# Optimization experiments

Measured on AMD Instinct MI355X. Metric: run time of the kernel, lower is better.

## Reference

```python
import jax, jax.numpy as jnp
import numpy as np

B, V, T, F, H = 32, 16, 64, 64, 512
NBINS = 36  # 360 / delta (delta_cog = delta_rb = 10)
OUT = 4     # output_size


def setup_inputs() -> dict:
    key = jax.random.key(0)
    ks = jax.random.split(key, 12)
    s = 1.0 / np.sqrt(H)
    return {
        'sequence': jax.random.normal(ks[0], (B, V, T, F), jnp.float32),
        'dist_matrix': jax.random.uniform(ks[1], (B, V, T, V), jnp.float32),
        'rb_matrix': jax.random.randint(ks[2], (B, V, T, V), 0, NBINS).astype(jnp.int32),
        'cog_matrix': jax.random.randint(ks[3], (B, V, T, V), 0, NBINS).astype(jnp.int32),
        'seq_mask': jnp.ones((B, V, T), jnp.float32),
        'maxval': jax.random.uniform(ks[4], (B, F), jnp.float32) + 1.0,
        'minval': jax.random.uniform(ks[5], (B, F), jnp.float32),
        # per-vessel LSTMCell params (PyTorch gate order i,f,g,o stacked along 4H)
        'W_ih': jax.random.normal(ks[6], (V, 4 * H, F), jnp.float32) * s,
        'W_hh': jax.random.normal(ks[7], (V, 4 * H, H), jnp.float32) * s,
        'b_ih': jnp.zeros((V, 4 * H), jnp.float32),
        'b_hh': jnp.zeros((V, 4 * H), jnp.float32),
        # hardwired attention domain table [360/delta_cog, 360/delta_rb]
        'domain': jax.random.normal(ks[8], (NBINS, NBINS), jnp.float32),
        # per-vessel softAttention linear (2H -> H)
        'soft_W': jax.random.normal(ks[9], (V, H, 2 * H), jnp.float32) * s,
        'soft_b': jnp.zeros((V, H), jnp.float32),
        # shared output linear (H -> F)
        'out_W': jax.random.normal(ks[10], (F, H), jnp.float32) * s,
        'out_b': jnp.zeros((F,), jnp.float32),
    }


def _forward(sequence, dist_matrix, rb_matrix, cog_matrix, seq_mask, maxval, minval,
             W_ih, W_hh, b_ih, b_hh, domain, soft_W, soft_b, out_W, out_b):
    B_, V_, T_, F_ = sequence.shape
    H_ = W_hh.shape[-1]

    def hardwired(h, r, d, m, cg):
        # h: [B,V,H]; r,d,cg: [B,V,V]; m: [B,V]
        mul1 = m[:, :, None] * m[:, None, :]
        mul2 = domain[cg, r]
        w = jax.nn.relu(mul2 - d) * mul1
        w = w / jax.lax.stop_gradient(jnp.max(w))  # torch: weights /= weights.data.max()
        return jnp.einsum('bvw,bwh->bvh', w, h)

    def lstm_step(x, h, c):
        # vectorized over V independent LSTMCells
        g = (jnp.einsum('bvf,vgf->bvg', x, W_ih)
             + jnp.einsum('bvh,vgh->bvg', h, W_hh) + b_ih + b_hh)
        i, f, gg, o = jnp.split(g, 4, axis=-1)
        c_new = jax.nn.sigmoid(f) * c + jax.nn.sigmoid(i) * jnp.tanh(gg)
        h_new = jax.nn.sigmoid(o) * jnp.tanh(c_new)
        return h_new, c_new

    h0 = jnp.zeros((B_, V_, H_), sequence.dtype)
    c0 = jnp.zeros((B_, V_, H_), sequence.dtype)
    xs = (jnp.moveaxis(sequence, 2, 0), jnp.moveaxis(rb_matrix, 2, 0),
          jnp.moveaxis(dist_matrix, 2, 0), jnp.moveaxis(seq_mask, 2, 0),
          jnp.moveaxis(cog_matrix, 2, 0))

    def enc_step(carry, xt):
        h, c = carry
        x, r, d, m, cg = xt
        wh = hardwired(h, r, d, m, cg)
        h, c = lstm_step(x, wh, c)
        return (h, c), h

    (h, c), enc = jax.lax.scan(enc_step, (h0, c0), xs)
    enc = jnp.moveaxis(enc, 0, 2)  # encodedInput [B,V,T,H]

    # decoder, prediction step i=0 (prediction_length=1)
    wh = hardwired(h, rb_matrix[:, :, -1], dist_matrix[:, :, -1],
                   seq_mask[:, :, -1], cog_matrix[:, :, -1])
    # get_previous_sequence: denormalize under no_grad
    prev = jax.lax.stop_gradient(
        sequence[:, :, -1] * (maxval - minval)[:, None, :] + minval[:, None, :])
    h, c = lstm_step(prev, wh, c)

    # per-vessel softAttention
    score = jnp.einsum('bvth,bvh->bvt', enc, h)
    alpha = jax.nn.softmax(score * seq_mask, axis=-1)
    ctx = jnp.einsum('bvt,bvth->bvh', alpha, enc)
    # faithful to torch.stack((ctx, h)).view(B, 2H) memory-reinterpret per vessel
    z = jnp.moveaxis(jnp.stack([ctx, h], axis=0), 2, 0).reshape(V_, B_, 2 * H_)
    h = jnp.moveaxis(
        jnp.tanh(jnp.einsum('vbk,vhk->vbh', z, soft_W) + soft_b[:, None, :]), 0, 1)

    out = jax.nn.relu(jnp.einsum('bvh,fh->bvf', h, out_W) + out_b)
    return out[:, :, None, :OUT]  # [B, V, prediction_length=1, output_size]


def reference(sequence, dist_matrix, rb_matrix, cog_matrix, seq_mask, maxval, minval,
              W_ih, W_hh, b_ih, b_hh, domain, soft_W, soft_b, out_W, out_b,
              maxVessels=V):
    return _forward(sequence, dist_matrix, rb_matrix, cog_matrix, seq_mask,
                    maxval, minval, W_ih, W_hh, b_ih, b_hh, domain,
                    soft_W, soft_b, out_W, out_b)
```

## Files before the change

kernel.cpp:

```cpp
#include <hip/hip_runtime.h>
#include <math.h>

#define B 32
#define V 16
#define T 64
#define F 64
#define H 512
#define NB 36
#define G4H 2048

typedef unsigned short u16;
typedef unsigned long long ull;
typedef __attribute__((ext_vector_type(8))) short bf16x8;
typedef __attribute__((ext_vector_type(4))) float f32x4;

#define OFF_H0     0
#define OFF_H1     262144
#define OFF_C      524288
#define OFF_CNT    786432
#define OFF_WALL   794624
#define OFF_CTX    794624
#define OFF_HSOFT  1056768
#define OFF_WMAX   1318912
#define OFF_WHSTG  1318976
#define OFF_SEQSTG 1581120
#define OFF_WSTG   2646080
#define OFF_ENC    12083264

#define WHP 262144
#define WLDS_BYTES 147456

__device__ __forceinline__ float sigmoidf_(float x) { return 1.0f / (1.0f + __expf(-x)); }

__device__ __forceinline__ u16 f2bf(float f) {
    union { float f; unsigned u; } x; x.f = f;
    unsigned r = x.u + 0x7FFF + ((x.u >> 16) & 1);
    return (u16)(r >> 16);
}
__device__ __forceinline__ float bf2f(u16 u) {
    union { unsigned i; float f; } x; x.i = ((unsigned)u) << 16;
    return x.f;
}
__device__ __forceinline__ f32x4 mfma16(bf16x8 a, bf16x8 b, f32x4 c) {
    return __builtin_amdgcn_mfma_f32_16x16x32_bf16(a, b, c, 0, 0, 0);
}
__device__ __forceinline__ bf16x8 mk_bf16x8(ull lo, ull hi) {
    union { ull u[2]; bf16x8 v; } x; x.u[0] = lo; x.u[1] = hi; return x.v;
}
__device__ __forceinline__ bf16x8 mk_bf16x8q(uint4 q) {
    union { uint4 q; bf16x8 v; } x; x.q = q; return x.v;
}

__device__ __forceinline__ ull ld_agent(const ull* p) {
    return __hip_atomic_load((ull*)p, __ATOMIC_RELAXED, __HIP_MEMORY_SCOPE_AGENT);
}
__device__ __forceinline__ void st_agent(ull* p, ull x) {
    __hip_atomic_store(p, x, __ATOMIC_RELAXED, __HIP_MEMORY_SCOPE_AGENT);
}
__device__ __forceinline__ void st_agent_f(float* p, float x) {
    __hip_atomic_store(p, x, __ATOMIC_RELAXED, __HIP_MEMORY_SCOPE_AGENT);
}
__device__ __forceinline__ void st_agent_u32(unsigned* p, unsigned x) {
    __hip_atomic_store(p, x, __ATOMIC_RELAXED, __HIP_MEMORY_SCOPE_AGENT);
}
__device__ __forceinline__ unsigned ld_agent_u32(const unsigned* p) {
    return __hip_atomic_load((unsigned*)p, __ATOMIC_RELAXED, __HIP_MEMORY_SCOPE_AGENT);
}

__global__ void k_zero(float* __restrict__ p, int n) {
    int i = blockIdx.x * blockDim.x + threadIdx.x;
    if (i < n) p[i] = 0.0f;
}

__global__ __launch_bounds__(256) void k_hw_all(
    const float* __restrict__ dist, const int* __restrict__ rb,
    const int* __restrict__ cog, const float* __restrict__ mask,
    const float* __restrict__ domain, float* __restrict__ w_all,
    float* __restrict__ wmax_all) {
    int t = blockIdx.x;
    __shared__ float red[256];
    int tid = threadIdx.x;
    float lmax = 0.0f;
    for (int idx = tid; idx < B * V * V; idx += 256) {
        int b = idx >> 8;
        int rem = idx & 255;
        int i = rem >> 4, j = rem & 15;
        int base = ((b * V + i) * T + t) * V + j;
        float val = domain[cog[base] * NB + rb[base]] - dist[base];
        val = val > 0.0f ? val : 0.0f;
        val *= mask[(b * V + i) * T + t] * mask[(b * V + j) * T + t];
        w_all[t * (B * V * V) + idx] = val;
        lmax = fmaxf(lmax, val);
    }
    red[tid] = lmax;
    __syncthreads();
    for (int s = 128; s > 0; s >>= 1) {
        if (tid < s) red[tid] = fmaxf(red[tid], red[tid + s]);
        __syncthreads();
    }
    if (tid == 0) wmax_all[t] = red[0];
}

__global__ __launch_bounds__(256) void k_wconv(
    const float* __restrict__ W_ih, const float* __restrict__ W_hh,
    u16* __restrict__ Wstg) {
    int v = blockIdx.x, hk = blockIdx.y, ks = blockIdx.z;
    int tid = threadIdx.x;
#pragma unroll
    for (int s = 0; s < 2; ++s) {
        int slot = tid + s * 256;
        int nt = slot >> 6, lane = slot & 63;
        int g = nt >> 1, hh = nt & 1;
        int col = g * H + hk * 32 + hh * 16 + (lane & 15);
        int k = ks * 32 + ((lane >> 4) << 3);
        const float* src = (k < F) ? &W_ih[(v * G4H + col) * F + k]
                                   : &W_hh[(v * G4H + col) * H + (k - F)];
        float4 x0 = *(const float4*)src;
        float4 x1 = *(const float4*)(src + 4);
        union { u16 u[8]; uint4 q; } pk;
        pk.u[0] = f2bf(x0.x); pk.u[1] = f2bf(x0.y); pk.u[2] = f2bf(x0.z); pk.u[3] = f2bf(x0.w);
        pk.u[4] = f2bf(x1.x); pk.u[5] = f2bf(x1.y); pk.u[6] = f2bf(x1.z); pk.u[7] = f2bf(x1.w);
        *(uint4*)&Wstg[(size_t)((((v * 16 + hk) * 18 + ks) * 8 + nt) * 64 + lane) * 8] = pk.q;
    }
}

__global__ __launch_bounds__(256) void k_seqstg(
    const float* __restrict__ seq, const float* __restrict__ maxval,
    const float* __restrict__ minval, u16* __restrict__ seqstg) {
    int v = blockIdx.x, t = blockIdx.y;
    int tid = threadIdx.x;
    int mt = tid >> 7, ks = (tid >> 6) & 1, lane = tid & 63;
    int b = mt * 16 + (lane & 15);
    int f = ks * 32 + ((lane >> 4) << 3);
    union { u16 u[8]; uint4 q; } pk;
    if (t < T) {
        const float* sp = &seq[((b * V + v) * T + t) * F + f];
        float4 x0 = *(const float4*)sp, x1 = *(const float4*)(sp + 4);
        pk.u[0] = f2bf(x0.x); pk.u[1] = f2bf(x0.y); pk.u[2] = f2bf(x0.z); pk.u[3] = f2bf(x0.w);
        pk.u[4] = f2bf(x1.x); pk.u[5] = f2bf(x1.y); pk.u[6] = f2bf(x1.z); pk.u[7] = f2bf(x1.w);
    } else {
        const float* sp = &seq[((b * V + v) * T + (T - 1)) * F + f];
        float4 x0 = *(const float4*)sp, x1 = *(const float4*)(sp + 4);
        float4 mx0 = *(const float4*)&maxval[b * F + f], mx1 = *(const float4*)&maxval[b * F + f + 4];
        float4 mn0 = *(const float4*)&minval[b * F + f], mn1 = *(const float4*)&minval[b * F + f + 4];
        pk.u[0] = f2bf(x0.x * (mx0.x - mn0.x) + mn0.x);
        pk.u[1] = f2bf(x0.y * (mx0.y - mn0.y) + mn0.y);
        pk.u[2] = f2bf(x0.z * (mx0.z - mn0.z) + mn0.z);
        pk.u[3] = f2bf(x0.w * (mx0.w - mn0.w) + mn0.w);
        pk.u[4] = f2bf(x1.x * (mx1.x - mn1.x) + mn1.x);
        pk.u[5] = f2bf(x1.y * (mx1.y - mn1.y) + mn1.y);
        pk.u[6] = f2bf(x1.z * (mx1.z - mn1.z) + mn1.z);
        pk.u[7] = f2bf(x1.w * (mx1.w - mn1.w) + mn1.w);
    }
    *(uint4*)&seqstg[(((size_t)(t * 16 + v)) * 4 + mt * 2 + ks) * 512 + lane * 8] = pk.q;
}

__global__ __launch_bounds__(256) void k_recur(
    const u16* __restrict__ seqstg, const u16* __restrict__ Wstg,
    const float* __restrict__ w_all, const float* __restrict__ wmax_all,
    const float* __restrict__ b_ih, const float* __restrict__ b_hh,
    float* __restrict__ h0buf, float* __restrict__ h1buf,
    float* __restrict__ c, u16* __restrict__ enc, u16* __restrict__ whstg,
    unsigned* __restrict__ bar) {
    extern __shared__ u16 Wlds[];

    int bid = blockIdx.x;
    int v = bid & 15, hk = bid >> 4;
    int tid = threadIdx.x;

    {
        const uint4* wsrc = (const uint4*)(Wstg + (size_t)((v * 16 + hk) * 18) * 4096);
        uint4* wdst = (uint4*)Wlds;
        for (int i = tid; i < 9216; i += 256) wdst[i] = wsrc[i];
    }

    int lane = tid & 63, wvi = tid >> 6;
    int mtw = wvi & 1, hh = wvi >> 1;
    int col = hk * 32 + hh * 16 + (lane & 15);
    int q4 = (lane >> 4) << 2;
    float bi = b_ih[v * G4H + col] + b_hh[v * G4H + col];
    float bf_ = b_ih[v * G4H + H + col] + b_hh[v * G4H + H + col];
    float bg_ = b_ih[v * G4H + 2 * H + col] + b_hh[v * G4H + 2 * H + col];
    float bo = b_ih[v * G4H + 3 * H + col] + b_hh[v * G4H + 3 * H + col];

    unsigned* aslot = bar + (v * 16 + hk) * 16;
    unsigned* bslot = bar + (256 + hk * 16 + v) * 16;
    unsigned* apoll = bar + (v * 16 + (tid & 15)) * 16;
    unsigned* bpoll = bar + (256 + hk * 16 + (tid & 15)) * 16;

    int a_b = tid >> 3;
    int a_cq = tid & 7;
    const int wh_idx = ((((v * 2 + (a_b >> 4)) * 16 + hk) * 64 +
                         (((a_cq >> 1) << 4) + (a_b & 15))) * 8 + (a_cq & 1) * 4);

    __syncthreads();

    for (int t = 0; t <= T; ++t) {
        int par = t & 1;
        int tm = t < T ? t : (T - 1);
        const float* hin = (t & 1) ? h0buf : h1buf;
        float* hout = (t & 1) ? h1buf : h0buf;

        uint4 s0 = *(const uint4*)&seqstg[(((size_t)(t * 16 + v)) * 4 + mtw * 2 + 0) * 512 + lane * 8];
        uint4 s1 = *(const uint4*)&seqstg[(((size_t)(t * 16 + v)) * 4 + mtw * 2 + 1) * 512 + lane * 8];
        float inv = 1.0f / wmax_all[tm];
        const float* wrow = &w_all[(size_t)tm * (B * V * V) + (a_b * V + v) * V];
        float4 wr0 = *(const float4*)(wrow);
        float4 wr1 = *(const float4*)(wrow + 4);
        float4 wr2 = *(const float4*)(wrow + 8);
        float4 wr3 = *(const float4*)(wrow + 12);
        float cprev[4];
#pragma unroll
        for (int r = 0; r < 4; ++r)
            cprev[r] = c[((mtw * 16 + q4 + r) * V + v) * H + col];

        f32x4 acc[4];
        acc[0][0] = bi;  acc[0][1] = bi;  acc[0][2] = bi;  acc[0][3] = bi;
        acc[1][0] = bf_; acc[1][1] = bf_; acc[1][2] = bf_; acc[1][3] = bf_;
        acc[2][0] = bg_; acc[2][1] = bg_; acc[2][2] = bg_; acc[2][3] = bg_;
        acc[3][0] = bo;  acc[3][1] = bo;  acc[3][2] = bo;  acc[3][3] = bo;
        {
            bf16x8 a0f = mk_bf16x8q(s0);
            bf16x8 a1f = mk_bf16x8q(s1);
#pragma unroll
            for (int g = 0; g < 4; ++g)
                acc[g] = mfma16(a0f, *(const bf16x8*)&Wlds[(0 * 8 + (g * 2 + hh)) * 512 + lane * 8], acc[g]);
#pragma unroll
            for (int g = 0; g < 4; ++g)
                acc[g] = mfma16(a1f, *(const bf16x8*)&Wlds[(1 * 8 + (g * 2 + hh)) * 512 + lane * 8], acc[g]);
        }

        if (t > 0) {
            if (tid < 16) {
                while (ld_agent_u32(bpoll) < (unsigned)t) __builtin_amdgcn_s_sleep(1);
            }
            __syncthreads();
        }

        {
            const ull* hb = (const ull*)&hin[(a_b * V) * H + hk * 32 + a_cq * 4];
            float a0 = 0.f, a1 = 0.f, a2 = 0.f, a3 = 0.f;
            const float wj[16] = {wr0.x, wr0.y, wr0.z, wr0.w, wr1.x, wr1.y, wr1.z, wr1.w,
                                  wr2.x, wr2.y, wr2.z, wr2.w, wr3.x, wr3.y, wr3.z, wr3.w};
#pragma unroll
            for (int j = 0; j < 16; ++j) {
                ull lo = ld_agent(hb + (size_t)j * (H / 2));
                ull hi = ld_agent(hb + (size_t)j * (H / 2) + 1);
                union { ull u; float f[2]; } u0, u1;
                u0.u = lo; u1.u = hi;
                a0 = fmaf(wj[j], u0.f[0], a0);
                a1 = fmaf(wj[j], u0.f[1], a1);
                a2 = fmaf(wj[j], u1.f[0], a2);
                a3 = fmaf(wj[j], u1.f[1], a3);
            }
            union { u16 u[4]; ull q; } pk;
            pk.u[0] = f2bf(a0 * inv); pk.u[1] = f2bf(a1 * inv);
            pk.u[2] = f2bf(a2 * inv); pk.u[3] = f2bf(a3 * inv);
            st_agent((ull*)&whstg[par * WHP + wh_idx], pk.q);
        }
        __syncthreads();
        if (tid == 0) st_agent_u32(aslot, (unsigned)(t + 1));

        if (tid < 16) {
            while (ld_agent_u32(apoll) < (unsigned)(t + 1)) __builtin_amdgcn_s_sleep(1);
        }
        __syncthreads();

        bf16x8 afr[16];
#pragma unroll
        for (int ksw = 0; ksw < 16; ++ksw) {
            const ull* src = (const ull*)&whstg[par * WHP + (((v * 2 + mtw) * 16 + ksw) * 64 + lane) * 8];
            ull lo = ld_agent(src), hi = ld_agent(src + 1);
            afr[ksw] = mk_bf16x8(lo, hi);
        }
#pragma unroll
        for (int ks = 0; ks < 16; ++ks) {
#pragma unroll
            for (int g = 0; g < 4; ++g) {
                bf16x8 wfr = *(const bf16x8*)&Wlds[((ks + 2) * 8 + (g * 2 + hh)) * 512 + lane * 8];
                acc[g] = mfma16(afr[ks], wfr, acc[g]);
            }
        }

        float cnv[4], hnv[4];
#pragma unroll
        for (int r = 0; r < 4; ++r) {
            float gi = acc[0][r];
            float gf = acc[1][r];
            float gg = acc[2][r];
            float go = acc[3][r];
            cnv[r] = sigmoidf_(gf) * cprev[r] + sigmoidf_(gi) * tanhf(gg);
            hnv[r] = sigmoidf_(go) * tanhf(cnv[r]);
            int b = mtw * 16 + q4 + r;
            st_agent_f(&hout[(b * V + v) * H + col], hnv[r]);
        }
        if (t < T) {
            __syncthreads();
            if (tid == 0) st_agent_u32(bslot, (unsigned)(t + 1));
        }

#pragma unroll
        for (int r = 0; r < 4; ++r) {
            int b = mtw * 16 + q4 + r;
            c[((b * V + v)) * H + col + 0 * H * V] = cnv[r];
            if (t < T) enc[((size_t)(b * V + v) * T + t) * H + col] = f2bf(hnv[r]);
        }
    }
}

__global__ __launch_bounds__(256) void k_attn(
    const u16* __restrict__ enc, const float* __restrict__ h,
    const float* __restrict__ mask, float* __restrict__ ctx) {
    int bid = blockIdx.x;
    int b = bid >> 4, v = bid & 15;
    int tid = threadIdx.x;
    int wave = tid >> 6, lane = tid & 63;
    __shared__ float hs[H];
    __shared__ float sc[T];
    __shared__ float al[T];
    const u16* encbase = enc + (size_t)((b * V + v) * T) * H;
    const float* hb = h + (b * V + v) * H;
    for (int i = tid; i < H; i += 256) hs[i] = hb[i];
    __syncthreads();
    for (int tt = wave; tt < T; tt += 4) {
        const u16* e = encbase + tt * H;
        float p = 0.0f;
#pragma unroll
        for (int ii = 0; ii < 8; ++ii) p += bf2f(e[ii * 64 + lane]) * hs[ii * 64 + lane];
        for (int off = 32; off; off >>= 1) p += __shfl_down(p, off, 64);
        if (lane == 0) sc[tt] = p;
    }
    __syncthreads();
    if (tid < 64) {
        float m_t = mask[(b * V + v) * T + tid];
        float s = sc[tid] * m_t;
        float mx = s;
        for (int off = 32; off; off >>= 1) mx = fmaxf(mx, __shfl_xor(mx, off, 64));
        float e = __expf(s - mx);
        float sum = e;
        for (int off = 32; off; off >>= 1) sum += __shfl_xor(sum, off, 64);
        al[tid] = e / sum;
    }
    __syncthreads();
    for (int hh = tid; hh < H; hh += 256) {
        float a = 0.0f;
        for (int tt = 0; tt < T; ++tt) a += al[tt] * bf2f(encbase[tt * H + hh]);
        ctx[(b * V + v) * H + hh] = a;
    }
}

__global__ __launch_bounds__(256) void k_soft(
    const float* __restrict__ ctx, const float* __restrict__ hdec,
    const float* __restrict__ soft_W, const float* __restrict__ soft_b,
    float* __restrict__ hsoft) {
    int v = blockIdx.x;
    int h0 = blockIdx.y * 32;
    int tid = threadIdx.x;
    int cg = tid & 31, rg = tid >> 5;
    __shared__ float sA[32][36];
    __shared__ float sW2[32][36];
    float* sAf = &sA[0][0];
    float* sWf = &sW2[0][0];
    float acc[4] = {0.f, 0.f, 0.f, 0.f};
    int arow = tid >> 3, akq = tid & 7;
    float4 areg, wreg;

    {
        int k = akq * 4;
        const float* src = (arow < 16) ? ctx : hdec;
        int bsrc = 2 * (arow & 15) + (k >= H ? 1 : 0);
        areg = *(const float4*)&src[(bsrc * V + v) * H + (k & (H - 1))];
        wreg = *(const float4*)&soft_W[(v * H + h0 + arow) * (2 * H) + k];
    }
    for (int kc = 0; kc < 2 * H; kc += 32) {
        __syncthreads();
        *(float4*)&sAf[arow * 36 + akq * 4] = areg;
        *(float4*)&sWf[arow * 36 + akq * 4] = wreg;
        __syncthreads();
        if (kc + 32 < 2 * H) {
            int k = kc + 32 + akq * 4;
            const float* src = (arow < 16) ? ctx : hdec;
            int bsrc = 2 * (arow & 15) + (k >= H ? 1 : 0);
            areg = *(const float4*)&src[(bsrc * V + v) * H + (k & (H - 1))];
            wreg = *(const float4*)&soft_W[(v * H + h0 + arow) * (2 * H) + kc + 32 + akq * 4];
        }
#pragma unroll
        for (int k4 = 0; k4 < 8; ++k4) {
            float4 wv = *(const float4*)&sWf[cg * 36 + k4 * 4];
            float4 a0 = *(const float4*)&sAf[(rg * 4 + 0) * 36 + k4 * 4];
            float4 a1 = *(const float4*)&sAf[(rg * 4 + 1) * 36 + k4 * 4];
            float4 a2 = *(const float4*)&sAf[(rg * 4 + 2) * 36 + k4 * 4];
            float4 a3 = *(const float4*)&sAf[(rg * 4 + 3) * 36 + k4 * 4];
            acc[0] += a0.x * wv.x + a0.y * wv.y + a0.z * wv.z + a0.w * wv.w;
            acc[1] += a1.x * wv.x + a1.y * wv.y + a1.z * wv.z + a1.w * wv.w;
            acc[2] += a2.x * wv.x + a2.y * wv.y + a2.z * wv.z + a2.w * wv.w;
            acc[3] += a3.x * wv.x + a3.y * wv.y + a3.z * wv.z + a3.w * wv.w;
        }
    }
    float bb = soft_b[v * H + h0 + cg];
#pragma unroll
    for (int r = 0; r < 4; ++r) {
        int row = rg * 4 + r;
        hsoft[(row * V + v) * H + h0 + cg] = tanhf(acc[r] + bb);
    }
}

__global__ __launch_bounds__(64) void k_out(
    const float* __restrict__ hsoft, const float* __restrict__ outW,
    const float* __restrict__ outb, float* __restrict__ out) {
    int bid = blockIdx.x;
    int b = bid >> 4, v = bid & 15;
    int lane = threadIdx.x;
    const float* hb = hsoft + (b * V + v) * H;
    float p[4] = {0.0f, 0.0f, 0.0f, 0.0f};
#pragma unroll
    for (int ii = 0; ii < 8; ++ii) {
        float hv = hb[ii * 64 + lane];
#pragma unroll
        for (int o = 0; o < 4; ++o) p[o] += hv * outW[o * H + ii * 64 + lane];
    }
#pragma unroll
    for (int o = 0; o < 4; ++o) {
        float s = p[o];
        for (int off = 32; off; off >>= 1) s += __shfl_down(s, off, 64);
        if (lane == 0) {
            float val = s + outb[o];
            out[(b * V + v) * 4 + o] = val > 0.0f ? val : 0.0f;
        }
    }
}

extern "C" void kernel_launch(void* const* d_in, const int* in_sizes, int n_in,
                              void* d_out, int out_size, void* d_ws, size_t ws_size,
                              hipStream_t stream) {
    const float* seq = (const float*)d_in[0];
    const float* dist = (const float*)d_in[1];
    const int* rb = (const int*)d_in[2];
    const int* cog = (const int*)d_in[3];
    const float* mask = (const float*)d_in[4];
    const float* maxval = (const float*)d_in[5];
    const float* minval = (const float*)d_in[6];
    const float* W_ih = (const float*)d_in[7];
    const float* W_hh = (const float*)d_in[8];
    const float* b_ih = (const float*)d_in[9];
    const float* b_hh = (const float*)d_in[10];
    const float* domain = (const float*)d_in[11];
    const float* soft_W = (const float*)d_in[12];
    const float* soft_b = (const float*)d_in[13];
    const float* out_W = (const float*)d_in[14];
    const float* out_b = (const float*)d_in[15];

    float* ws = (float*)d_ws;
    float* h0buf = ws + OFF_H0;
    float* h1buf = ws + OFF_H1;
    float* c = ws + OFF_C;
    unsigned* bar = (unsigned*)(ws + OFF_CNT);
    float* w_all = ws + OFF_WALL;
    float* ctx = ws + OFF_CTX;
    float* hsoft = ws + OFF_HSOFT;
    float* wmax_all = ws + OFF_WMAX;
    u16* whstg = (u16*)(ws + OFF_WHSTG);
    u16* seqstg = (u16*)(ws + OFF_SEQSTG);
    u16* Wstg = (u16*)(ws + OFF_WSTG);
    u16* enc = (u16*)(ws + OFF_ENC);

    (void)hipFuncSetAttribute((const void*)k_recur,
                              hipFuncAttributeMaxDynamicSharedMemorySize, WLDS_BYTES);

    k_zero<<<3104, 256, 0, stream>>>(ws, 794624);
    k_hw_all<<<T, 256, 0, stream>>>(dist, rb, cog, mask, domain, w_all, wmax_all);
    k_wconv<<<dim3(16, 16, 18), 256, 0, stream>>>(W_ih, W_hh, Wstg);
    k_seqstg<<<dim3(16, T + 1), 256, 0, stream>>>(seq, maxval, minval, seqstg);

    k_recur<<<256, 256, WLDS_BYTES, stream>>>(seqstg, Wstg, w_all, wmax_all,
                                              b_ih, b_hh, h0buf, h1buf, c, enc,
                                              whstg, bar);

    k_attn<<<B * V, 256, 0, stream>>>(enc, h0buf, mask, ctx);
    k_soft<<<dim3(16, 16), 256, 0, stream>>>(ctx, h0buf, soft_W, soft_b, hsoft);
    k_out<<<B * V, 64, 0, stream>>>(hsoft, out_W, out_b, (float*)d_out);
}
```

Baseline: 720.3 us.

## Replace block-wide barriers with per-wave flags and merge prep kernels

The recurrent kernel's cross-block synchronisation is reworked. Each wave now publishes its own progress flag and polls only the flags of the specific producer waves it depends on, with half a wave spinning. This replaces the block-level __syncthreads plus single-thread flag and sleeping poll, shortening the per-timestep dependency chain across the 64 steps. Separately, the four preprocessing launches (zeroing, hardwired weights, weight conversion, sequence staging) are fused into one launch to cut launch overhead. The flag area is enlarged and workspace offsets shift. Busy-spinning without sleep may add memory traffic, and correctness now relies on s_waitcnt ordering within each wave.

```diff
diff --git a/kernel.cpp b/kernel.cpp
--- a/kernel.cpp
+++ b/kernel.cpp
@@ -18,17 +18,18 @@
 #define OFF_H1     262144
 #define OFF_C      524288
 #define OFF_CNT    786432
-#define OFF_WALL   794624
-#define OFF_CTX    794624
-#define OFF_HSOFT  1056768
-#define OFF_WMAX   1318912
-#define OFF_WHSTG  1318976
-#define OFF_SEQSTG 1581120
-#define OFF_WSTG   2646080
-#define OFF_ENC    12083264
+#define OFF_WALL   819200
+#define OFF_CTX    819200
+#define OFF_HSOFT  1081344
+#define OFF_WMAX   1343488
+#define OFF_WHSTG  1343552
+#define OFF_SEQSTG 1605696
+#define OFF_WSTG   2670656
+#define OFF_ENC    12107840
 
 #define WHP 262144
 #define WLDS_BYTES 147456
+#define HFLAG_BASE 16384
 
 __device__ __forceinline__ float sigmoidf_(float x) { return 1.0f / (1.0f + __expf(-x)); }
 
@@ -67,92 +68,100 @@
     return __hip_atomic_load((unsigned*)p, __ATOMIC_RELAXED, __HIP_MEMORY_SCOPE_AGENT);
 }
 
-__global__ void k_zero(float* __restrict__ p, int n) {
-    int i = blockIdx.x * blockDim.x + threadIdx.x;
-    if (i < n) p[i] = 0.0f;
-}
-
-__global__ __launch_bounds__(256) void k_hw_all(
+#define NZB 3200
+#define NHW 64
+#define NWC 4608
+#define NSS 1040
+__global__ __launch_bounds__(256) void k_prep(
+    float* __restrict__ ws,
     const float* __restrict__ dist, const int* __restrict__ rb,
     const int* __restrict__ cog, const float* __restrict__ mask,
     const float* __restrict__ domain, float* __restrict__ w_all,
-    float* __restrict__ wmax_all) {
-    int t = blockIdx.x;
-    __shared__ float red[256];
-    int tid = threadIdx.x;
-    float lmax = 0.0f;
-    for (int idx = tid; idx < B * V * V; idx += 256) {
-        int b = idx >> 8;
-        int rem = idx & 255;
-        int i = rem >> 4, j = rem & 15;
-        int base = ((b * V + i) * T + t) * V + j;
-        float val = domain[cog[base] * NB + rb[base]] - dist[base];
-        val = val > 0.0f ? val : 0.0f;
-        val *= mask[(b * V + i) * T + t] * mask[(b * V + j) * T + t];
-        w_all[t * (B * V * V) + idx] = val;
-        lmax = fmaxf(lmax, val);
-    }
-    red[tid] = lmax;
-    __syncthreads();
-    for (int s = 128; s > 0; s >>= 1) {
-        if (tid < s) red[tid] = fmaxf(red[tid], red[tid + s]);
-        __syncthreads();
-    }
-    if (tid == 0) wmax_all[t] = red[0];
-}
-
-__global__ __launch_bounds__(256) void k_wconv(
+    float* __restrict__ wmax_all,
     const float* __restrict__ W_ih, const float* __restrict__ W_hh,
-    u16* __restrict__ Wstg) {
-    int v = blockIdx.x, hk = blockIdx.y, ks = blockIdx.z;
-    int tid = threadIdx.x;
-#pragma unroll
-    for (int s = 0; s < 2; ++s) {
-        int slot = tid + s * 256;
-        int nt = slot >> 6, lane = slot & 63;
-        int g = nt >> 1, hh = nt & 1;
-        int col = g * H + hk * 32 + hh * 16 + (lane & 15);
-        int k = ks * 32 + ((lane >> 4) << 3);
-        const float* src = (k < F) ? &W_ih[(v * G4H + col) * F + k]
-                                   : &W_hh[(v * G4H + col) * H + (k - F)];
-        float4 x0 = *(const float4*)src;
-        float4 x1 = *(const float4*)(src + 4);
-        union { u16 u[8]; uint4 q; } pk;
-        pk.u[0] = f2bf(x0.x); pk.u[1] = f2bf(x0.y); pk.u[2] = f2bf(x0.z); pk.u[3] = f2bf(x0.w);
-        pk.u[4] = f2bf(x1.x); pk.u[5] = f2bf(x1.y); pk.u[6] = f2bf(x1.z); pk.u[7] = f2bf(x1.w);
-        *(uint4*)&Wstg[(size_t)((((v * 16 + hk) * 18 + ks) * 8 + nt) * 64 + lane) * 8] = pk.q;
-    }
-}
-
-__global__ __launch_bounds__(256) void k_seqstg(
+    u16* __restrict__ Wstg,
     const float* __restrict__ seq, const float* __restrict__ maxval,
     const float* __restrict__ minval, u16* __restrict__ seqstg) {
-    int v = blockIdx.x, t = blockIdx.y;
+    __shared__ float red[256];
+    int bid = blockIdx.x;
     int tid = threadIdx.x;
-    int mt = tid >> 7, ks = (tid >> 6) & 1, lane = tid & 63;
-    int b = mt * 16 + (lane & 15);
-    int f = ks * 32 + ((lane >> 4) << 3);
-    union { u16 u[8]; uint4 q; } pk;
-    if (t < T) {
-        const float* sp = &seq[((b * V + v) * T + t) * F + f];
-        float4 x0 = *(const float4*)sp, x1 = *(const float4*)(sp + 4);
-        pk.u[0] = f2bf(x0.x); pk.u[1] = f2bf(x0.y); pk.u[2] = f2bf(x0.z); pk.u[3] = f2bf(x0.w);
-        pk.u[4] = f2bf(x1.x); pk.u[5] = f2bf(x1.y); pk.u[6] = f2bf(x1.z); pk.u[7] = f2bf(x1.w);
-    } else {
-        const float* sp = &seq[((b * V + v) * T + (T - 1)) * F + f];
-        float4 x0 = *(const float4*)sp, x1 = *(const float4*)(sp + 4);
-        float4 mx0 = *(const float4*)&maxval[b * F + f], mx1 = *(const float4*)&maxval[b * F + f + 4];
-        float4 mn0 = *(const float4*)&minval[b * F + f], mn1 = *(const float4*)&minval[b * F + f + 4];
-        pk.u[0] = f2bf(x0.x * (mx0.x - mn0.x) + mn0.x);
-        pk.u[1] = f2bf(x0.y * (mx0.y - mn0.y) + mn0.y);
-        pk.u[2] = f2bf(x0.z * (mx0.z - mn0.z) + mn0.z);
-        pk.u[3] = f2bf(x0.w * (mx0.w - mn0.w) + mn0.w);
-        pk.u[4] = f2bf(x1.x * (mx1.x - mn1.x) + mn1.x);
-        pk.u[5] = f2bf(x1.y * (mx1.y - mn1.y) + mn1.y);
-        pk.u[6] = f2bf(x1.z * (mx1.z - mn1.z) + mn1.z);
-        pk.u[7] = f2bf(x1.w * (mx1.w - mn1.w) + mn1.w);
-    }
-    *(uint4*)&seqstg[(((size_t)(t * 16 + v)) * 4 + mt * 2 + ks) * 512 + lane * 8] = pk.q;
+
+    if (bid < NZB) {
+        ws[bid * 256 + tid] = 0.0f;
+        return;
+    }
+    if (bid < NZB + NHW) {
+        int t = bid - NZB;
+        float lmax = 0.0f;
+        for (int idx = tid; idx < B * V * V; idx += 256) {
+            int b = idx >> 8;
+            int rem = idx & 255;
+            int i = rem >> 4, j = rem & 15;
+            int base = ((b * V + i) * T + t) * V + j;
+            float val = domain[cog[base] * NB + rb[base]] - dist[base];
+            val = val > 0.0f ? val : 0.0f;
+            val *= mask[(b * V + i) * T + t] * mask[(b * V + j) * T + t];
+            w_all[t * (B * V * V) + idx] = val;
+            lmax = fmaxf(lmax, val);
+        }
+        red[tid] = lmax;
+        __syncthreads();
+        for (int s = 128; s > 0; s >>= 1) {
+            if (tid < s) red[tid] = fmaxf(red[tid], red[tid + s]);
+            __syncthreads();
+        }
+        if (tid == 0) wmax_all[t] = red[0];
+        return;
+    }
+    if (bid < NZB + NHW + NWC) {
+        int idx = bid - (NZB + NHW);
+        int v = idx / 288, hk = (idx / 18) & 15, ks = idx % 18;
+#pragma unroll
+        for (int s = 0; s < 2; ++s) {
+            int slot = tid + s * 256;
+            int nt = slot >> 6, lane = slot & 63;
+            int g = nt >> 1, hh = nt & 1;
+            int col = g * H + hk * 32 + hh * 16 + (lane & 15);
+            int k = ks * 32 + ((lane >> 4) << 3);
+            const float* src = (k < F) ? &W_ih[(v * G4H + col) * F + k]
+                                       : &W_hh[(v * G4H + col) * H + (k - F)];
+            float4 x0 = *(const float4*)src;
+            float4 x1 = *(const float4*)(src + 4);
+            union { u16 u[8]; uint4 q; } pk;
+            pk.u[0] = f2bf(x0.x); pk.u[1] = f2bf(x0.y); pk.u[2] = f2bf(x0.z); pk.u[3] = f2bf(x0.w);
+            pk.u[4] = f2bf(x1.x); pk.u[5] = f2bf(x1.y); pk.u[6] = f2bf(x1.z); pk.u[7] = f2bf(x1.w);
+            *(uint4*)&Wstg[(size_t)((((v * 16 + hk) * 18 + ks) * 8 + nt) * 64 + lane) * 8] = pk.q;
+        }
+        return;
+    }
+    {
+        int idx = bid - (NZB + NHW + NWC);
+        int v = idx / 65, t = idx % 65;
+        int mt = tid >> 7, ks = (tid >> 6) & 1, lane = tid & 63;
+        int b = mt * 16 + (lane & 15);
+        int f = ks * 32 + ((lane >> 4) << 3);
+        union { u16 u[8]; uint4 q; } pk;
+        if (t < T) {
+            const float* sp = &seq[((b * V + v) * T + t) * F + f];
+            float4 x0 = *(const float4*)sp, x1 = *(const float4*)(sp + 4);
+            pk.u[0] = f2bf(x0.x); pk.u[1] = f2bf(x0.y); pk.u[2] = f2bf(x0.z); pk.u[3] = f2bf(x0.w);
+            pk.u[4] = f2bf(x1.x); pk.u[5] = f2bf(x1.y); pk.u[6] = f2bf(x1.z); pk.u[7] = f2bf(x1.w);
+        } else {
+            const float* sp = &seq[((b * V + v) * T + (T - 1)) * F + f];
+            float4 x0 = *(const float4*)sp, x1 = *(const float4*)(sp + 4);
+            float4 mx0 = *(const float4*)&maxval[b * F + f], mx1 = *(const float4*)&maxval[b * F + f + 4];
+            float4 mn0 = *(const float4*)&minval[b * F + f], mn1 = *(const float4*)&minval[b * F + f + 4];
+            pk.u[0] = f2bf(x0.x * (mx0.x - mn0.x) + mn0.x);
+            pk.u[1] = f2bf(x0.y * (mx0.y - mn0.y) + mn0.y);
+            pk.u[2] = f2bf(x0.z * (mx0.z - mn0.z) + mn0.z);
+            pk.u[3] = f2bf(x0.w * (mx0.w - mn0.w) + mn0.w);
+            pk.u[4] = f2bf(x1.x * (mx1.x - mn1.x) + mn1.x);
+            pk.u[5] = f2bf(x1.y * (mx1.y - mn1.y) + mn1.y);
+            pk.u[6] = f2bf(x1.z * (mx1.z - mn1.z) + mn1.z);
+            pk.u[7] = f2bf(x1.w * (mx1.w - mn1.w) + mn1.w);
+        }
+        *(uint4*)&seqstg[(((size_t)(t * 16 + v)) * 4 + mt * 2 + ks) * 512 + lane * 8] = pk.q;
+    }
 }
 
 __global__ __launch_bounds__(256) void k_recur(
@@ -174,8 +183,8 @@
         for (int i = tid; i < 9216; i += 256) wdst[i] = wsrc[i];
     }
 
-    int lane = tid & 63, wvi = tid >> 6;
-    int mtw = wvi & 1, hh = wvi >> 1;
+    int lane = tid & 63, w = tid >> 6;
+    int mtw = w & 1, hh = w >> 1;
     int col = hk * 32 + hh * 16 + (lane & 15);
     int q4 = (lane >> 4) << 2;
     float bi = b_ih[v * G4H + col] + b_hh[v * G4H + col];
@@ -183,10 +192,12 @@
     float bg_ = b_ih[v * G4H + 2 * H + col] + b_hh[v * G4H + 2 * H + col];
     float bo = b_ih[v * G4H + 3 * H + col] + b_hh[v * G4H + 3 * H + col];
 
-    unsigned* aslot = bar + (v * 16 + hk) * 16;
-    unsigned* bslot = bar + (256 + hk * 16 + v) * 16;
-    unsigned* apoll = bar + (v * 16 + (tid & 15)) * 16;
-    unsigned* bpoll = bar + (256 + hk * 16 + (tid & 15)) * 16;
+    unsigned* a_sig = bar + (bid * 4 + w) * 16;
+    unsigned* h_sig = bar + HFLAG_BASE + (bid * 4 + w) * 16;
+    unsigned* h_poll = bar + HFLAG_BASE +
+        (((hk * 16 + (lane >> 1)) * 4) + ((w >> 1) + (lane & 1) * 2)) * 16;
+    unsigned* a_poll = bar +
+        ((((lane >> 1) * 16 + v) * 4) + (2 * mtw + (lane & 1))) * 16;
 
     int a_b = tid >> 3;
     int a_cq = tid & 7;
@@ -231,10 +242,10 @@
         }
 
         if (t > 0) {
-            if (tid < 16) {
-                while (ld_agent_u32(bpoll) < (unsigned)t) __builtin_amdgcn_s_sleep(1);
+            if (lane < 32) {
+                while (ld_agent_u32(h_poll) < (unsigned)t) {}
             }
-            __syncthreads();
+            __builtin_amdgcn_sched_barrier(0);
         }
 
         {
@@ -258,13 +269,14 @@
             pk.u[2] = f2bf(a2 * inv); pk.u[3] = f2bf(a3 * inv);
             st_agent((ull*)&whstg[par * WHP + wh_idx], pk.q);
         }
-        __syncthreads();
-        if (tid == 0) st_agent_u32(aslot, (unsigned)(t + 1));
-
-        if (tid < 16) {
-            while (ld_agent_u32(apoll) < (unsigned)(t + 1)) __builtin_amdgcn_s_sleep(1);
-        }
-        __syncthreads();
+        __builtin_amdgcn_s_waitcnt(0);
+        __builtin_amdgcn_sched_barrier(0);
+        if (lane == 0) st_agent_u32(a_sig, (unsigned)(t + 1));
+
+        if (lane < 32) {
+            while (ld_agent_u32(a_poll) < (unsigned)(t + 1)) {}
+        }
+        __builtin_amdgcn_sched_barrier(0);
 
         bf16x8 afr[16];
 #pragma unroll
@@ -295,14 +307,15 @@
             st_agent_f(&hout[(b * V + v) * H + col], hnv[r]);
         }
         if (t < T) {
-            __syncthreads();
-            if (tid == 0) st_agent_u32(bslot, (unsigned)(t + 1));
+            __builtin_amdgcn_s_waitcnt(0);
+            __builtin_amdgcn_sched_barrier(0);
+            if (lane == 0) st_agent_u32(h_sig, (unsigned)(t + 1));
         }
 
 #pragma unroll
         for (int r = 0; r < 4; ++r) {
             int b = mtw * 16 + q4 + r;
-            c[((b * V + v)) * H + col + 0 * H * V] = cnv[r];
+            c[(b * V + v) * H + col] = cnv[r];
             if (t < T) enc[((size_t)(b * V + v) * T + t) * H + col] = f2bf(hnv[r]);
         }
     }
@@ -467,10 +480,9 @@
     (void)hipFuncSetAttribute((const void*)k_recur,
                               hipFuncAttributeMaxDynamicSharedMemorySize, WLDS_BYTES);
 
-    k_zero<<<3104, 256, 0, stream>>>(ws, 794624);
-    k_hw_all<<<T, 256, 0, stream>>>(dist, rb, cog, mask, domain, w_all, wmax_all);
-    k_wconv<<<dim3(16, 16, 18), 256, 0, stream>>>(W_ih, W_hh, Wstg);
-    k_seqstg<<<dim3(16, T + 1), 256, 0, stream>>>(seq, maxval, minval, seqstg);
+    k_prep<<<NZB + NHW + NWC + NSS, 256, 0, stream>>>(
+        ws, dist, rb, cog, mask, domain, w_all, wmax_all,
+        W_ih, W_hh, Wstg, seq, maxval, minval, seqstg);
 
     k_recur<<<256, 256, WLDS_BYTES, stream>>>(seqstg, Wstg, w_all, wmax_all,
                                               b_ih, b_hh, h0buf, h1buf, c, enc,
```

Result: slower. 809.5 us (+12.4%).
